# Optimization experiments

Measured on AMD Instinct MI355X. Metric: run time of the kernel, lower is better.

## Reference

```python
import jax, jax.numpy as jnp
import numpy as np

OUT, IN = 4096, 4096
GROUP_SIZE = 128
NUMEL = OUT * IN                 # 16,777,216 int4 values
N_GROUPS = NUMEL // GROUP_SIZE   # 131,072
N_PACKED = NUMEL // 2            # 8,388,608 bytes (stored as int32 0..255)


def _dequantize_int4(q_packed, q_scales, q_zeros):
    """Unpack two 4-bit values per byte, dequant per group, reshape to (OUT, IN)."""
    low = q_packed & 0xF                     # [N_PACKED]
    high = (q_packed >> 4) & 0xF             # [N_PACKED]
    # interleave: flat[2i] = low nibble, flat[2i+1] = high nibble
    q = jnp.stack([low, high], axis=-1).reshape(NUMEL)            # [NUMEL] int
    qg = q.astype(jnp.float32).reshape(N_GROUPS, GROUP_SIZE)      # [G, group]
    w = (qg - q_zeros[:, None]) * q_scales[:, None]
    return w.reshape(OUT, IN)


def setup_inputs() -> dict:
    key = jax.random.key(0)
    k = jax.random.split(key, 6)
    x = jax.random.normal(k[0], (4, 2048, IN), dtype=jnp.float32)
    q_packed = jax.random.randint(k[1], (N_PACKED,), 0, 256, dtype=jnp.int32)
    q_scales = jax.random.uniform(k[2], (N_GROUPS,), dtype=jnp.float32) * 0.02 + 1e-3
    q_zeros = jax.random.uniform(k[3], (N_GROUPS,), dtype=jnp.float32) * 15.0
    delta_weight = jax.random.normal(k[4], (OUT, IN), dtype=jnp.float32) * 0.01
    bias = jax.random.normal(k[5], (OUT,), dtype=jnp.float32)
    return {"x": x, "q_packed": q_packed, "q_scales": q_scales,
            "q_zeros": q_zeros, "delta_weight": delta_weight, "bias": bias}


def reference(x, q_packed, q_scales, q_zeros, delta_weight, bias):
    W = _dequantize_int4(q_packed, q_scales, q_zeros)   # [OUT, IN]
    W_eff = W + delta_weight
    # F.linear: y = x @ W_eff^T + bias
    h = jnp.einsum('bsi,oi->bso', x, W_eff) + bias
    return h
```

## Files before the change

### kernel.cpp

```cpp
#include <hip/hip_runtime.h>


#define M_DIM 8192
#define N_DIM 4096
#define K_DIM 4096
#define NUMEL (N_DIM * K_DIM)

typedef _Float16 half_t;
typedef __attribute__((ext_vector_type(4))) _Float16 half4v;
typedef __attribute__((ext_vector_type(8))) _Float16 half8v;
typedef __attribute__((ext_vector_type(8))) short short8v;
typedef __attribute__((ext_vector_type(8))) unsigned short ushort8v;
typedef __attribute__((ext_vector_type(4))) float float4v;
typedef __attribute__((ext_vector_type(4))) int int4v;

#define KTILES 64
#define LDT 72

static __device__ __forceinline__ void gload16(const void* g, void* l) {
    __builtin_amdgcn_global_load_lds(
        (const __attribute__((address_space(1))) void*)g,
        (__attribute__((address_space(3))) void*)l, 16, 0, 0);
}

static __device__ __forceinline__ unsigned short f2bf(float f) {
    unsigned u = __builtin_bit_cast(unsigned, f);
    u += 0x7fffu + ((u >> 16) & 1u);
    return (unsigned short)(u >> 16);
}

__global__ __launch_bounds__(256) void k_pack_w(
    const int* __restrict__ qp, const float* __restrict__ sc,
    const float* __restrict__ zr, const float* __restrict__ dwt,
    unsigned char* __restrict__ Wp)
{
    const size_t o = ((size_t)blockIdx.x * 256 + threadIdx.x) << 4;
    const int chunk16 = (int)(o >> 14);
    const int c  = (int)(o >> 10) & 15;
    const int ln = (int)(o >> 4) & 63;
    const int n = (chunk16 >> 6) * 128 + (c >> 1) * 16 + (ln & 15);
    const int k = (chunk16 & 63) * 64 + (c & 1) * 32 + (ln >> 4) * 8;
    const long flat = (long)n * K_DIM + k;
    const int g = n * 32 + (k >> 7);
    const float s = sc[g];
    const float zs = zr[g] * s;
    int4v q4 = *(const int4v*)(qp + (flat >> 1));
    float4v d0 = *(const float4v*)(dwt + flat);
    float4v d1 = *(const float4v*)(dwt + flat + 4);
    float d[8] = {d0[0], d0[1], d0[2], d0[3], d1[0], d1[1], d1[2], d1[3]};
    ushort8v vh;
#pragma unroll
    for (int j = 0; j < 4; ++j) {
        vh[2*j]   = f2bf(fmaf((float)(q4[j] & 15),        s, d[2*j]   - zs));
        vh[2*j+1] = f2bf(fmaf((float)((q4[j] >> 4) & 15), s, d[2*j+1] - zs));
    }
    *(ushort8v*)(Wp + o) = vh;
}

__global__ __launch_bounds__(256) void k_pack_x(
    const float* __restrict__ X, unsigned char* __restrict__ Xp)
{
    const size_t o = ((size_t)blockIdx.x * 256 + threadIdx.x) << 4;
    const int chunk16 = (int)(o >> 14);
    const int c  = (int)(o >> 10) & 15;
    const int ln = (int)(o >> 4) & 63;
    const int m = (chunk16 >> 6) * 128 + (c >> 1) * 16 + (ln & 15);
    const int k = (chunk16 & 63) * 64 + (c & 1) * 32 + (ln >> 4) * 8;
    const float* src = X + (size_t)m * K_DIM + k;
    float4v x0 = *(const float4v*)(src);
    float4v x1 = *(const float4v*)(src + 4);
    ushort8v vh;
    vh[0] = f2bf(x0[0]); vh[1] = f2bf(x0[1]);
    vh[2] = f2bf(x0[2]); vh[3] = f2bf(x0[3]);
    vh[4] = f2bf(x1[0]); vh[5] = f2bf(x1[1]);
    vh[6] = f2bf(x1[2]); vh[7] = f2bf(x1[3]);
    *(ushort8v*)(Xp + o) = vh;
}

#define BARX() do { __builtin_amdgcn_sched_barrier(0); \
                    __builtin_amdgcn_s_barrier(); \
                    __builtin_amdgcn_sched_barrier(0); } while(0)
#define WAITV(N) do { asm volatile("s_waitcnt vmcnt(" #N ")" ::: "memory"); \
                      __builtin_amdgcn_sched_barrier(0); } while(0)

#define READ_A(BUF, F0) do { \
_Pragma("unroll") for (int i_ = 0; i_ < 4; ++i_) \
_Pragma("unroll") for (int ks_ = 0; ks_ < 2; ++ks_) \
        ah[i_][ks_] = *(const short8v*)(&lds[BUF][wm] \
            [((((F0) + i_) * 2 + ks_) << 10) + lane16]); \
    } while(0)

#define READ_B(BUF, DST, J0) do { \
_Pragma("unroll") for (int j_ = 0; j_ < 2; ++j_) \
_Pragma("unroll") for (int ks_ = 0; ks_ < 2; ++ks_) \
        DST[j_][ks_] = *(const short8v*)(&lds[BUF][bhalf] \
            [bq8192 + ((((J0) + j_) * 2 + ks_) << 10) + lane16]); \
    } while(0)

#define MFMA_Q(F0, N0, BREG) do { \
    __builtin_amdgcn_s_setprio(1); \
_Pragma("unroll") for (int i_ = 0; i_ < 4; ++i_) \
_Pragma("unroll") for (int j_ = 0; j_ < 2; ++j_) \
_Pragma("unroll") for (int ks_ = 0; ks_ < 2; ++ks_) \
        acc[(F0)+i_][(N0)+j_] = __builtin_amdgcn_mfma_f32_16x16x32_bf16( \
            ah[i_][ks_], BREG[j_][ks_], acc[(F0)+i_][(N0)+j_], 0, 0, 0); \
    __builtin_amdgcn_s_setprio(0); \
} while(0)

__global__ __launch_bounds__(512, 2) void k_gemm8ph(
    const unsigned char* __restrict__ Apk, const unsigned char* __restrict__ Bpk,
    const float* __restrict__ bias, float* __restrict__ Y)
{
    __shared__ __align__(16) unsigned char lds[2][4][16384];

    const int tid  = threadIdx.x;
    const int lane = tid & 63;
    const int wave = tid >> 6;
    const int wm = wave >> 2;
    const int wn = wave & 3;
    const int bhalf = 2 + (wn >> 1);
    const int bq8192 = (wn & 1) << 13;
    const int lane16 = lane << 4;

    const int wg = blockIdx.x;
    const int swg = (wg & 7) * 64 + (wg >> 3);
    const int bn = swg & 15;
    const int bm = swg >> 4;

    auto asrc = [&](int h, int tk) {
        return Apk + ((((size_t)(2 * bm + h)) * KTILES + tk) << 14);
    };
    auto bsrc = [&](int h, int tk) {
        return Bpk + ((((size_t)(2 * bn + h)) * KTILES + tk) << 14);
    };
    auto stageh = [&](int b, int h, const unsigned char* s) {
        unsigned char* d = &lds[b][h][tid << 4];
        gload16(s + (tid << 4), d);
        gload16(s + 8192 + (tid << 4), d + 8192);
    };

    short8v ah[4][2], b01[2][2], b23[2][2];
    float4v acc[8][4];
    const float4v zero4 = {0.f, 0.f, 0.f, 0.f};
#pragma unroll
    for (int i = 0; i < 8; ++i)
#pragma unroll
        for (int j = 0; j < 4; ++j) acc[i][j] = zero4;

    stageh(0, 0, asrc(0, 0)); stageh(0, 1, asrc(1, 0));
    stageh(0, 2, bsrc(0, 0)); stageh(0, 3, bsrc(1, 0));
    stageh(1, 2, bsrc(0, 1)); stageh(1, 3, bsrc(1, 1));
    WAITV(4);
    BARX();

    for (int it = 0; it < 31; ++it) {
        const int t1 = 2 * it + 1, t2 = 2 * it + 2, t3 = 2 * it + 3;
        READ_A(0, 0); READ_B(0, b01, 0);
        stageh(1, 0, asrc(0, t1)); stageh(1, 1, asrc(1, t1));
        MFMA_Q(0, 0, b01);
        READ_B(0, b23, 2);
        MFMA_Q(0, 2, b23);
        READ_A(0, 4);
        BARX();
        MFMA_Q(4, 2, b23);
        stageh(0, 2, bsrc(0, t2)); stageh(0, 3, bsrc(1, t2));
        WAITV(4);
        BARX();
        MFMA_Q(4, 0, b01);
        READ_A(1, 0); READ_B(1, b01, 0);
        stageh(0, 0, asrc(0, t2)); stageh(0, 1, asrc(1, t2));
        MFMA_Q(0, 0, b01);
        READ_B(1, b23, 2);
        MFMA_Q(0, 2, b23);
        READ_A(1, 4);
        BARX();
        MFMA_Q(4, 2, b23);
        stageh(1, 2, bsrc(0, t3)); stageh(1, 3, bsrc(1, t3));
        WAITV(4);
        BARX();
        MFMA_Q(4, 0, b01);
    }

    READ_A(0, 0); READ_B(0, b01, 0);
    stageh(1, 0, asrc(0, 63)); stageh(1, 1, asrc(1, 63));
    BARX(); MFMA_Q(0, 0, b01);
    READ_B(0, b23, 2);
    BARX(); MFMA_Q(0, 2, b23);
    READ_A(0, 4);
    BARX(); MFMA_Q(4, 2, b23);
    WAITV(0);
    BARX(); MFMA_Q(4, 0, b01);
    READ_A(1, 0); READ_B(1, b01, 0);
    BARX(); MFMA_Q(0, 0, b01);
    READ_B(1, b23, 2);
    BARX(); MFMA_Q(0, 2, b23);
    READ_A(1, 4);
    BARX(); MFMA_Q(4, 2, b23);
    MFMA_Q(4, 0, b01);

    const long m0 = (long)bm * 256 + wm * 128;
    const long n0 = (long)bn * 256 + wn * 64;
#pragma unroll
    for (int mf = 0; mf < 8; ++mf) {
        const long row = m0 + mf * 16 + (lane >> 4) * 4;
#pragma unroll
        for (int nf = 0; nf < 4; ++nf) {
            const long col = n0 + nf * 16 + (lane & 15);
            const float b = bias[col];
#pragma unroll
            for (int r = 0; r < 4; ++r)
                Y[(row + r) * N_DIM + col] = acc[mf][nf][r] + b;
        }
    }
}

__global__ __launch_bounds__(256, 2) void k_gemm_fused(
    const float* __restrict__ X, const int* __restrict__ qp,
    const float* __restrict__ sc, const float* __restrict__ zr,
    const float* __restrict__ dwt,
    const float* __restrict__ bias, float* __restrict__ Y)
{
    __shared__ __align__(16) half_t Ah[128 * LDT];
    __shared__ __align__(16) half_t Bh[128 * LDT];

    const int tid  = threadIdx.x;
    const int lane = tid & 63;
    const int wave = tid >> 6;
    const int wm = wave >> 1, wn = wave & 1;
    const int bn = blockIdx.x & 31;
    const int bm = blockIdx.x >> 5;
    const long m0 = (long)bm * 128;
    const long n0 = (long)bn * 128;
    const int fr = lane & 15;
    const int ko = (lane >> 4) * 8;

    const float4v zero4 = {0.f, 0.f, 0.f, 0.f};
    float4v acc[4][4];
#pragma unroll
    for (int i = 0; i < 4; ++i)
#pragma unroll
        for (int j = 0; j < 4; ++j) acc[i][j] = zero4;

    for (int k0 = 0; k0 < K_DIM; k0 += 64) {
        {
            const int ar = tid >> 4;
            const int ac = (tid & 15) * 4;
#pragma unroll
            for (int rr = 0; rr < 8; ++rr) {
                const int row = ar + rr * 16;
                float4v xv = *(const float4v*)(X + (m0 + row) * K_DIM + k0 + ac);
                half4v h;
#pragma unroll
                for (int j = 0; j < 4; ++j) h[j] = (half_t)xv[j];
                *(half4v*)(Ah + row * LDT + ac) = h;
            }
        }
        {
            const int cr = tid >> 3;
            const int cc = (tid & 7) * 8;
#pragma unroll
            for (int rr = 0; rr < 4; ++rr) {
                const int row = cr + rr * 32;
                const long n = n0 + row;
                const int g = (int)(n * 32 + (k0 >> 7));
                const float s = sc[g];
                const float zs = zr[g] * s;
                const long flat = n * K_DIM + k0 + cc;
                int4v q4 = *(const int4v*)(qp + (flat >> 1));
                float4v d0 = *(const float4v*)(dwt + flat);
                float4v d1 = *(const float4v*)(dwt + flat + 4);
                float d[8] = {d0[0], d0[1], d0[2], d0[3], d1[0], d1[1], d1[2], d1[3]};
                half8v vh;
#pragma unroll
                for (int j = 0; j < 4; ++j) {
                    vh[2*j]   = (half_t)fmaf((float)(q4[j] & 15),        s, d[2*j]   - zs);
                    vh[2*j+1] = (half_t)fmaf((float)((q4[j] >> 4) & 15), s, d[2*j+1] - zs);
                }
                *(half8v*)(Bh + row * LDT + cc) = vh;
            }
        }
        __syncthreads();
#pragma unroll
        for (int ks = 0; ks < 2; ++ks) {
            const int kk = ks * 32 + ko;
            half8v a2[4], b2[4];
#pragma unroll
            for (int i = 0; i < 4; ++i) {
                a2[i] = *(const half8v*)(Ah + (wm * 64 + i * 16 + fr) * LDT + kk);
                b2[i] = *(const half8v*)(Bh + (wn * 64 + i * 16 + fr) * LDT + kk);
            }
#pragma unroll
            for (int i = 0; i < 4; ++i)
#pragma unroll
                for (int j = 0; j < 4; ++j)
                    acc[i][j] = __builtin_amdgcn_mfma_f32_16x16x32_f16(
                        a2[i], b2[j], acc[i][j], 0, 0, 0);
        }
        __syncthreads();
    }

#pragma unroll
    for (int i = 0; i < 4; ++i) {
        const long mrow = m0 + wm * 64 + i * 16 + (lane >> 4) * 4;
#pragma unroll
        for (int j = 0; j < 4; ++j) {
            const long col = n0 + wn * 64 + j * 16 + (lane & 15);
            const float b = bias[col];
#pragma unroll
            for (int r = 0; r < 4; ++r)
                Y[(mrow + r) * N_DIM + col] = acc[i][j][r] + b;
        }
    }
}

extern "C" void kernel_launch(void* const* d_in, const int* in_sizes, int n_in,
                              void* d_out, int out_size, void* d_ws, size_t ws_size,
                              hipStream_t stream)
{
    const float* X  = (const float*)d_in[0];
    const int*   qp = (const int*)d_in[1];
    const float* sc = (const float*)d_in[2];
    const float* zr = (const float*)d_in[3];
    const float* dwt = (const float*)d_in[4];
    const float* bs = (const float*)d_in[5];
    float* Y = (float*)d_out;

    const size_t needB = (size_t)N_DIM * K_DIM * 2;
    const size_t needA = (size_t)M_DIM * K_DIM * 2;

    if (ws_size >= needA + needB) {
        unsigned char* Bpk = (unsigned char*)d_ws;
        unsigned char* Apk = Bpk + needB;
        k_pack_w<<<dim3((unsigned)(needB >> 12)), dim3(256), 0, stream>>>(qp, sc, zr, dwt, Bpk);
        k_pack_x<<<dim3((unsigned)(needA >> 12)), dim3(256), 0, stream>>>(X, Apk);
        k_gemm8ph<<<dim3((M_DIM / 256) * (N_DIM / 256)), dim3(512), 0, stream>>>(Apk, Bpk, bs, Y);
    } else {
        k_gemm_fused<<<dim3((M_DIM / 128) * (N_DIM / 128)), dim3(256), 0, stream>>>(
            X, qp, sc, zr, dwt, bs, Y);
    }
}
```

Measured before the change: 268.4 us.

## Load B fragments directly from global into registers, quad-buffer A in LDS

The GEMM no longer stages B in LDS. Each wave loads its pre-packed B fragments straight from global memory into registers, double-buffered one k-tile ahead, while the A tile is staged in a four-deep LDS ring with prefetch distance two. This drops the B LDS writes and reads and lets the main loop use one barrier per k-tile instead of two. In exchange it needs more VGPRs for the B buffers, and global-load latency now sits directly on the MFMA register operands, so vmcnt waits could stall if the prefetch is not deep enough.

Result: slower. 286.1 us (+6.6%).

```diff
diff --git a/kernel.cpp b/kernel.cpp
--- a/kernel.cpp
+++ b/kernel.cpp
@@ -80,22 +80,40 @@
 #define BARX() do { __builtin_amdgcn_sched_barrier(0); \
                     __builtin_amdgcn_s_barrier(); \
                     __builtin_amdgcn_sched_barrier(0); } while(0)
-#define WAITV(N) do { asm volatile("s_waitcnt vmcnt(" #N ")" ::: "memory"); \
-                      __builtin_amdgcn_sched_barrier(0); } while(0)
+#define WAITV_(N) do { __builtin_amdgcn_sched_barrier(0); \
+                       asm volatile("s_waitcnt vmcnt(" #N ")" ::: "memory"); \
+                       __builtin_amdgcn_sched_barrier(0); } while(0)
+#define WAITV(N) WAITV_(N)
+
+#define STAGE_A(BUF, T) do { \
+    const unsigned char* s0_ = ap0 + ((size_t)(T) << 14); \
+    const unsigned char* s1_ = ap1 + ((size_t)(T) << 14); \
+    gload16(s0_,        &lds4[BUF][t16]); \
+    gload16(s0_ + 8192, &lds4[BUF][t16 + 8192]); \
+    gload16(s1_,        &lds4[BUF][16384 + t16]); \
+    gload16(s1_ + 8192, &lds4[BUF][16384 + t16 + 8192]); \
+} while(0)
+
+#define LOADB01(SET, T) do { \
+_Pragma("unroll") for (int j_ = 0; j_ < 2; ++j_) \
+_Pragma("unroll") for (int ks_ = 0; ks_ < 2; ++ks_) \
+        SET[j_][ks_] = *(const short8v*)(bgl + ((size_t)(T) << 14) \
+                                             + ((j_ * 2 + ks_) << 10)); \
+} while(0)
+
+#define LOADB23(T) do { \
+_Pragma("unroll") for (int j_ = 0; j_ < 2; ++j_) \
+_Pragma("unroll") for (int ks_ = 0; ks_ < 2; ++ks_) \
+        b23[j_][ks_] = *(const short8v*)(bgl + ((size_t)(T) << 14) \
+                                             + (((2 + j_) * 2 + ks_) << 10)); \
+} while(0)
 
 #define READ_A(BUF, F0) do { \
 _Pragma("unroll") for (int i_ = 0; i_ < 4; ++i_) \
 _Pragma("unroll") for (int ks_ = 0; ks_ < 2; ++ks_) \
-        ah[i_][ks_] = *(const short8v*)(&lds[BUF][wm] \
-            [((((F0) + i_) * 2 + ks_) << 10) + lane16]); \
-    } while(0)
-
-#define READ_B(BUF, DST, J0) do { \
-_Pragma("unroll") for (int j_ = 0; j_ < 2; ++j_) \
-_Pragma("unroll") for (int ks_ = 0; ks_ < 2; ++ks_) \
-        DST[j_][ks_] = *(const short8v*)(&lds[BUF][bhalf] \
-            [bq8192 + ((((J0) + j_) * 2 + ks_) << 10) + lane16]); \
-    } while(0)
+        ah[i_][ks_] = *(const short8v*)(&lds4[BUF] \
+            [awm + ((((F0) + i_) * 2 + ks_) << 10) + lane16]); \
+} while(0)
 
 #define MFMA_Q(F0, N0, BREG) do { \
     __builtin_amdgcn_s_setprio(1); \
@@ -107,39 +125,47 @@
     __builtin_amdgcn_s_setprio(0); \
 } while(0)
 
-__global__ __launch_bounds__(512, 2) void k_gemm8ph(
+#define BODY(RBUF, SBUF, BCUR, BNXT, T, STG, LDB, WVN) do { \
+    if (STG) { STAGE_A(SBUF, (T) + 2); } \
+    __builtin_amdgcn_sched_barrier(0); \
+    if (LDB) { LOADB01(BNXT, (T) + 1); } \
+    READ_A(RBUF, 0); \
+    MFMA_Q(0, 0, BCUR); \
+    MFMA_Q(0, 2, b23); \
+    READ_A(RBUF, 4); \
+    MFMA_Q(4, 2, b23); \
+    if (LDB) { LOADB23((T) + 1); } \
+    MFMA_Q(4, 0, BCUR); \
+    WAITV(WVN); \
+    BARX(); \
+} while(0)
+
+__global__ __launch_bounds__(512, 2) void k_gemm_breg(
     const unsigned char* __restrict__ Apk, const unsigned char* __restrict__ Bpk,
     const float* __restrict__ bias, float* __restrict__ Y)
 {
-    __shared__ __align__(16) unsigned char lds[2][4][16384];
+    __shared__ __align__(16) unsigned char lds4[4][32768];
 
     const int tid  = threadIdx.x;
     const int lane = tid & 63;
     const int wave = tid >> 6;
     const int wm = wave >> 2;
     const int wn = wave & 3;
-    const int bhalf = 2 + (wn >> 1);
-    const int bq8192 = (wn & 1) << 13;
     const int lane16 = lane << 4;
+    const int t16 = tid << 4;
+    const int awm = wm << 14;
 
     const int wg = blockIdx.x;
     const int swg = (wg & 7) * 64 + (wg >> 3);
     const int bn = swg & 15;
     const int bm = swg >> 4;
 
-    auto asrc = [&](int h, int tk) {
-        return Apk + ((((size_t)(2 * bm + h)) * KTILES + tk) << 14);
-    };
-    auto bsrc = [&](int h, int tk) {
-        return Bpk + ((((size_t)(2 * bn + h)) * KTILES + tk) << 14);
-    };
-    auto stageh = [&](int b, int h, const unsigned char* s) {
-        unsigned char* d = &lds[b][h][tid << 4];
-        gload16(s + (tid << 4), d);
-        gload16(s + 8192 + (tid << 4), d + 8192);
-    };
-
-    short8v ah[4][2], b01[2][2], b23[2][2];
+    const unsigned char* ap0 = Apk + (((size_t)(2 * bm)     * KTILES) << 14) + t16;
+    const unsigned char* ap1 = Apk + (((size_t)(2 * bm + 1) * KTILES) << 14) + t16;
+    const unsigned char* bgl = Bpk + (((size_t)(2 * bn + (wn >> 1)) * KTILES) << 14)
+                             + ((wn & 1) << 13) + lane16;
+
+    short8v ah[4][2], b01A[2][2], b01B[2][2], b23[2][2];
     float4v acc[8][4];
     const float4v zero4 = {0.f, 0.f, 0.f, 0.f};
 #pragma unroll
@@ -147,56 +173,30 @@
 #pragma unroll
         for (int j = 0; j < 4; ++j) acc[i][j] = zero4;
 
-    stageh(0, 0, asrc(0, 0)); stageh(0, 1, asrc(1, 0));
-    stageh(0, 2, bsrc(0, 0)); stageh(0, 3, bsrc(1, 0));
-    stageh(1, 2, bsrc(0, 1)); stageh(1, 3, bsrc(1, 1));
-    WAITV(4);
+    STAGE_A(0, 0);
+    STAGE_A(1, 1);
+    __builtin_amdgcn_sched_barrier(0);
+    LOADB01(b01A, 0);
+    LOADB23(0);
+    WAITV(12);
     BARX();
 
-    for (int it = 0; it < 31; ++it) {
-        const int t1 = 2 * it + 1, t2 = 2 * it + 2, t3 = 2 * it + 3;
-        READ_A(0, 0); READ_B(0, b01, 0);
-        stageh(1, 0, asrc(0, t1)); stageh(1, 1, asrc(1, t1));
-        MFMA_Q(0, 0, b01);
-        READ_B(0, b23, 2);
-        MFMA_Q(0, 2, b23);
-        READ_A(0, 4);
-        BARX();
-        MFMA_Q(4, 2, b23);
-        stageh(0, 2, bsrc(0, t2)); stageh(0, 3, bsrc(1, t2));
-        WAITV(4);
-        BARX();
-        MFMA_Q(4, 0, b01);
-        READ_A(1, 0); READ_B(1, b01, 0);
-        stageh(0, 0, asrc(0, t2)); stageh(0, 1, asrc(1, t2));
-        MFMA_Q(0, 0, b01);
-        READ_B(1, b23, 2);
-        MFMA_Q(0, 2, b23);
-        READ_A(1, 4);
-        BARX();
-        MFMA_Q(4, 2, b23);
-        stageh(1, 2, bsrc(0, t3)); stageh(1, 3, bsrc(1, t3));
-        WAITV(4);
-        BARX();
-        MFMA_Q(4, 0, b01);
-    }
-
-    READ_A(0, 0); READ_B(0, b01, 0);
-    stageh(1, 0, asrc(0, 63)); stageh(1, 1, asrc(1, 63));
-    BARX(); MFMA_Q(0, 0, b01);
-    READ_B(0, b23, 2);
-    BARX(); MFMA_Q(0, 2, b23);
-    READ_A(0, 4);
-    BARX(); MFMA_Q(4, 2, b23);
-    WAITV(0);
-    BARX(); MFMA_Q(4, 0, b01);
-    READ_A(1, 0); READ_B(1, b01, 0);
-    BARX(); MFMA_Q(0, 0, b01);
-    READ_B(1, b23, 2);
-    BARX(); MFMA_Q(0, 2, b23);
-    READ_A(1, 4);
-    BARX(); MFMA_Q(4, 2, b23);
-    MFMA_Q(4, 0, b01);
+    for (int it = 0; it < 15; ++it) {
+        const int t0 = it << 2;
+        BODY(0, 2, b01A, b01B, t0,     1, 1, 20);
+        BODY(1, 3, b01B, b01A, t0 + 1, 1, 1, 20);
+        BODY(2, 0, b01A, b01B, t0 + 2, 1, 1, 20);
+        BODY(3, 1, b01B, b01A, t0 + 3, 1, 1, 20);
+    }
+    BODY(0, 2, b01A, b01B, 60, 1, 1, 20);
+    BODY(1, 3, b01B, b01A, 61, 1, 1, 20);
+    BODY(2, 0, b01A, b01B, 62, 0, 1, 8);
+    READ_A(3, 0);
+    MFMA_Q(0, 0, b01B);
+    MFMA_Q(0, 2, b23);
+    READ_A(3, 4);
+    MFMA_Q(4, 2, b23);
+    MFMA_Q(4, 0, b01B);
 
     const long m0 = (long)bm * 256 + wm * 128;
     const long n0 = (long)bn * 256 + wn * 64;
@@ -333,7 +333,7 @@
         unsigned char* Apk = Bpk + needB;
         k_pack_w<<<dim3((unsigned)(needB >> 12)), dim3(256), 0, stream>>>(qp, sc, zr, dwt, Bpk);
         k_pack_x<<<dim3((unsigned)(needA >> 12)), dim3(256), 0, stream>>>(X, Apk);
-        k_gemm8ph<<<dim3((M_DIM / 256) * (N_DIM / 256)), dim3(512), 0, stream>>>(Apk, Bpk, bs, Y);
+        k_gemm_breg<<<dim3((M_DIM / 256) * (N_DIM / 256)), dim3(512), 0, stream>>>(Apk, Bpk, bs, Y);
     } else {
         k_gemm_fused<<<dim3((M_DIM / 128) * (N_DIM / 128)), dim3(256), 0, stream>>>(
             X, qp, sc, zr, dwt, bs, Y);
```
